# Kernel optimization log

Hardware: AMD Instinct MI355X
Metric: run time of the kernel (lower is better)

The kernel has to match this reference:

```python
import jax, jax.numpy as jnp
import numpy as np

B, S, T, H, F, V, OUT = 32, 40, 60, 256, 64, 50000, 128
D_IN = H + F  # LSTM input = input_size + feature_size (input_size == hidden_size)


def setup_inputs() -> dict:
    rng = np.random.default_rng(0)
    key = jax.random.key(0)
    ks = jax.random.split(key, 12)
    sc = 0.05
    # descending sentence counts per paragraph (pack_padded_sequence order), max == S
    lens = np.sort(rng.integers(1, S + 1, size=B))[::-1].copy()
    lens[0] = S
    # per-sentence token lengths; trailing (padding) sentences have length 0
    tok_len = rng.integers(1, T + 1, size=(B, S))
    tok_len = tok_len * (np.arange(S)[None, :] < lens[:, None])
    x_mask = jnp.asarray(np.arange(T)[None, None, :] >= tok_len[:, :, None])  # True = pad
    return {
        "x": jax.random.randint(ks[0], (B, S, T), 0, V),
        "x_mask": x_mask,
        "x_feature": jax.random.normal(ks[1], (B, S, T, F), jnp.float32),
        "sentences_len": jnp.asarray(lens, jnp.int32),
        "clause": jnp.zeros((B,), jnp.int32),
        "cls": jnp.zeros((B,), jnp.int32),
        "emb": jax.random.normal(ks[2], (V, H), jnp.float32) * 0.02,
        "attn_w": jax.random.normal(ks[3], (H,), jnp.float32) * sc,
        "attn_b": jnp.zeros((), jnp.float32),
        "wih_f": jax.random.normal(ks[4], (4 * H, D_IN), jnp.float32) * sc,
        "whh_f": jax.random.normal(ks[5], (4 * H, H), jnp.float32) * sc,
        "bih_f": jnp.zeros((4 * H,), jnp.float32),
        "bhh_f": jnp.zeros((4 * H,), jnp.float32),
        "wih_b": jax.random.normal(ks[6], (4 * H, D_IN), jnp.float32) * sc,
        "whh_b": jax.random.normal(ks[7], (4 * H, H), jnp.float32) * sc,
        "bih_b": jnp.zeros((4 * H,), jnp.float32),
        "bhh_b": jnp.zeros((4 * H,), jnp.float32),
        "fc_w": jax.random.normal(ks[8], (OUT, 2 * H), jnp.float32) * sc,
        "fc_b": jnp.zeros((OUT,), jnp.float32),
        "bn_gamma": jnp.ones((OUT,), jnp.float32),
        "bn_beta": jnp.zeros((OUT,), jnp.float32),
    }


def _lstm_last(X, m, wih, whh, bih, bhh, reverse):
    # X: (S, B, D) time-major inputs; m: (S, B) bool validity mask.
    # Masked update emulates pack_padded_sequence: carry freezes past each seq's length,
    # so the final carry equals torch's h_n for that direction.
    def step(carry, inp):
        h, c = carry
        xt, mt = inp
        g = xt @ wih.T + bih + h @ whh.T + bhh
        i, f, gg, o = jnp.split(g, 4, axis=-1)  # torch gate order i,f,g,o
        c2 = jax.nn.sigmoid(f) * c + jax.nn.sigmoid(i) * jnp.tanh(gg)
        h2 = jax.nn.sigmoid(o) * jnp.tanh(c2)
        upd = mt[:, None]
        return (jnp.where(upd, h2, h), jnp.where(upd, c2, c)), None

    nb, nh = X.shape[1], whh.shape[1]
    init = (jnp.zeros((nb, nh), X.dtype), jnp.zeros((nb, nh), X.dtype))
    (h, _), _ = jax.lax.scan(step, init, (X, m), reverse=reverse)
    return h


def _forward(x, x_mask, x_feature, sentences_len, emb, attn_w, attn_b,
             wih_f, whh_f, bih_f, bhh_f, wih_b, whh_b, bih_b, bhh_b,
             fc_w, fc_b, bn_gamma, bn_beta):
    e = emb[x]                                            # (B,S,T,H)
    valid_tok = ~x_mask                                   # (B,S,T)
    valid_sen = jnp.any(valid_tok, axis=-1)               # (B,S)
    score = jnp.einsum('bsth,h->bst', e, attn_w) + attn_b
    score = jnp.where(valid_tok, score, -jnp.inf)
    score = jnp.where(valid_sen[..., None], score, 0.0)   # avoid all-inf NaN rows
    alpha = jax.nn.relu(jax.nn.softmax(score, axis=-1))   # (B,S,T)
    alpha = jnp.where(valid_sen[..., None] & valid_tok, alpha, 0.0)
    emb_part = jnp.einsum('bst,bsth->bsh', alpha, e)      # attended sum over tokens
    feat_part = jnp.sum(x_feature * valid_tok[..., None].astype(x_feature.dtype), axis=2)
    sen = jnp.concatenate([emb_part, feat_part], axis=-1) # (B,S,H+F)
    sen = sen * valid_sen[..., None].astype(sen.dtype)    # empty sentences -> zero rows
    X = jnp.transpose(sen, (1, 0, 2))                     # (S,B,H+F) time-major
    m = jnp.arange(X.shape[0])[:, None] < sentences_len[None, :]  # (S,B)
    h_f = _lstm_last(X, m, wih_f, whh_f, bih_f, bhh_f, reverse=False)
    h_b = _lstm_last(X, m, wih_b, whh_b, bih_b, bhh_b, reverse=True)
    # torch: paragraph_hidden[0].view(batch, -1) on (2,B,H) = flat memory reinterpretation
    hidden = jnp.stack([h_f, h_b], axis=0).reshape(x.shape[0], -1)  # (B,2H)
    logits = hidden @ fc_w.T + fc_b                       # (B,OUT)
    mu = jnp.mean(logits, axis=0)
    var = jnp.mean((logits - mu) ** 2, axis=0)            # biased var (BN train mode)
    y = jax.nn.relu(bn_gamma * (logits - mu) / jnp.sqrt(var + 1e-5) + bn_beta)
    return jax.nn.log_softmax(y, axis=0)                  # original softmaxes over batch dim


def reference(x, x_mask, x_feature, sentences_len, clause, cls, emb, attn_w, attn_b,
              wih_f, whh_f, bih_f, bhh_f, wih_b, whh_b, bih_b, bhh_b,
              fc_w, fc_b, bn_gamma, bn_beta):
    # clause / cls are unused by the original forward
    return _forward(x, x_mask, x_feature, sentences_len, emb, attn_w, attn_b,
                    wih_f, whh_f, bih_f, bhh_f, wih_b, whh_b, bih_b, bhh_b,
                    fc_w, fc_b, bn_gamma, bn_beta)
```

## Files before the change

kernel.cpp:

```cpp
#include <hip/hip_runtime.h>
#include <stdint.h>

#define NB 32
#define NS 40
#define NT 60
#define NH 256
#define NF 64
#define NDIN 320
#define NG 1024
#define NSB 1280
#define NOUT 128

typedef __bf16 bf16x8 __attribute__((ext_vector_type(8)));
typedef float f32x4 __attribute__((ext_vector_type(4)));
typedef uint32_t u32x4 __attribute__((ext_vector_type(4)));

union bfrag { bf16x8 v; uint16_t u[8]; uint4 q; uint64_t d[2]; };
union f2arr { float2 v; float a[2]; };

__device__ __forceinline__ uint16_t f2bf(float f) {
  uint32_t u = __float_as_uint(f);
  u += 0x7fffu + ((u >> 16) & 1u);
  return (uint16_t)(u >> 16);
}
__device__ __forceinline__ float bf2f(uint16_t h) {
  return __uint_as_float(((uint32_t)h) << 16);
}
__device__ __forceinline__ float sig_fast(float x) { return 1.0f / (1.0f + __expf(-x)); }
__device__ __forceinline__ float tanh_fast(float x) {
  x = fminf(fmaxf(x, -15.0f), 15.0f);
  float t = __expf(2.0f * x);
  return (t - 1.0f) / (t + 1.0f);
}
__device__ __forceinline__ uint32_t ld_agent_u32(const uint32_t* p) {
  return __hip_atomic_load(p, __ATOMIC_RELAXED, __HIP_MEMORY_SCOPE_AGENT);
}

__global__ __launch_bounds__(256) void k_detect(const uint32_t* __restrict__ xm,
                                                int* __restrict__ flags,
                                                uint32_t* __restrict__ gr) {
  int bid = blockIdx.x, tid = threadIdx.x;
  {
    int gidx = bid * 256 + tid;
    u32x4 z = {0, 0, 0, 0};
    asm volatile("global_store_dwordx4 %0, %1, off sc1"
                 :: "v"((unsigned long long)(uintptr_t)(gr + (size_t)gidx * 4)), "v"(z)
                 : "memory");
  }
  __shared__ int s_notint, s_notflt;
  if (tid == 0) { s_notint = 0; s_notflt = 0; }
  __syncthreads();
  int notint = 0, notflt = 0;
  for (int i = bid * 600 + tid; i < (bid + 1) * 600; i += 256) {
    uint32_t v = xm[i];
    if (v > 1u) notint = 1;
    if (v != 0u && v != 0x3f800000u) notflt = 1;
  }
  if (notint) atomicOr(&s_notint, 1);
  if (notflt) atomicOr(&s_notflt, 1);
  __syncthreads();
  if (tid == 0) flags[8 + bid] = s_notint | (s_notflt << 1);
}

__global__ __launch_bounds__(256) void k_attn_prep(
    const int* __restrict__ x, const void* __restrict__ xmask,
    const float* __restrict__ xfeat, const int* __restrict__ slen,
    const float* __restrict__ emb, const float* __restrict__ attn_w,
    uint16_t* __restrict__ Xb, const int* __restrict__ flagp,
    const float* __restrict__ wf, const float* __restrict__ wb,
    uint16_t* __restrict__ outw)
{
  int tid = threadIdx.x;
  if (blockIdx.x >= 1280) {
    const int n = NG * NDIN;
    for (int idx = (blockIdx.x - 1280) * 256 + tid; idx < 2 * n; idx += 1280 * 256) {
      float v = (idx < n) ? wf[idx] : wb[idx - n];
      uint16_t hi = f2bf(v);
      outw[idx] = hi;
      outw[2 * n + idx] = f2bf(v - bf2f(hi));
    }
    return;
  }
  int bs = blockIdx.x;
  int b = bs / NS, s = bs % NS;
  uint16_t* Xh = Xb + (size_t)(s * NB + b) * NDIN;
  uint16_t* Xl = Xh + (size_t)NSB * NDIN;
  int len = slen[b];
  if (s >= len) {
    for (int i = tid; i < NDIN; i += 256) { Xh[i] = 0; Xl[i] = 0; }
    return;
  }
  __shared__ __attribute__((aligned(16))) float sw[NH];
  __shared__ float salpha[NT];
  __shared__ int sidx[NT];
  __shared__ unsigned char svalid[NT];
  __shared__ __attribute__((aligned(16))) uint16_t es[NT][NH];
  sw[tid] = attn_w[tid];
  int nv = 0;
  #pragma unroll
  for (int q = 0; q < 32; q++) nv |= flagp[8 + q];
  int flag = (!(nv & 1)) ? 0 : ((!(nv & 2)) ? 2 : 1);
  if (tid < NT) {
    int mi = bs * NT + tid;
    sidx[tid] = x[mi];
    int mv;
    if (flag == 1)      mv = ((const unsigned char*)xmask)[mi];
    else if (flag == 2) mv = (((const float*)xmask)[mi] != 0.0f) ? 1 : 0;
    else                mv = ((const int*)xmask)[mi];
    svalid[tid] = (mv == 0) ? 1 : 0;
  }
  __syncthreads();
  int wave = tid >> 6, lane = tid & 63;
  for (int t = wave; t < NT; t += 4) {
    float d = 0.0f;
    if (svalid[t]) {
      const float* er = emb + (size_t)sidx[t] * NH;
      float4 e4 = ((const float4*)er)[lane];
      float4 w4 = ((const float4*)sw)[lane];
      uint16_t* ed = &es[t][lane * 4];
      ed[0] = f2bf(e4.x); ed[1] = f2bf(e4.y); ed[2] = f2bf(e4.z); ed[3] = f2bf(e4.w);
      d = e4.x * w4.x + e4.y * w4.y + e4.z * w4.z + e4.w * w4.w;
      #pragma unroll
      for (int o = 32; o > 0; o >>= 1) d += __shfl_down(d, o);
    }
    if (lane == 0) salpha[t] = d;
  }
  __syncthreads();
  if (tid < 64) {
    int valid = (tid < NT) && svalid[tid];
    float v = valid ? salpha[tid] : -1e30f;
    float m = v;
    #pragma unroll
    for (int o = 32; o > 0; o >>= 1) m = fmaxf(m, __shfl_xor(m, o));
    float e = valid ? expf(v - m) : 0.0f;
    float ssum = e;
    #pragma unroll
    for (int o = 32; o > 0; o >>= 1) ssum += __shfl_xor(ssum, o);
    if (tid < NT) salpha[tid] = e / ssum;
  }
  __syncthreads();
  float acc = 0.0f;
  for (int t = 0; t < NT; t++) {
    float a = salpha[t];
    if (a != 0.0f) acc += a * bf2f(es[t][tid]);
  }
  {
    uint16_t hi = f2bf(acc);
    Xh[tid] = hi; Xl[tid] = f2bf(acc - bf2f(hi));
  }
  if (tid < NF) {
    float fa = 0.0f;
    const float* fp = xfeat + (size_t)bs * NT * NF + tid;
    for (int t = 0; t < NT; t++) if (svalid[t]) fa += fp[t * NF];
    uint16_t hi = f2bf(fa);
    Xh[NH + tid] = hi; Xl[NH + tid] = f2bf(fa - bf2f(hi));
  }
}

__global__ __launch_bounds__(512) void k_gbase(
    const uint16_t* __restrict__ Xb, const uint16_t* __restrict__ wihb,
    const float* __restrict__ bih_f, const float* __restrict__ bhh_f,
    const float* __restrict__ bih_b, const float* __restrict__ bhh_b,
    float* __restrict__ gbase)
{
  const int n = NG * NDIN;
  int wave = threadIdx.x >> 6, lane = threadIdx.x & 63;
  int job = blockIdx.x * 8 + wave;
  int dir = job / 1280;
  int r = job % 1280;
  int nt = r % 64, ms = r / 64;
  int m0 = ms * 64;
  const uint16_t* Wh = wihb + (size_t)dir * n;
  const uint16_t* Wl = Wh + (size_t)2 * n;
  const uint16_t* Ah = Xb;
  const uint16_t* Al = Xb + (size_t)NSB * NDIN;
  int lrow = lane & 15, lk = (lane >> 4) * 8;
  f32x4 acc0 = {0,0,0,0}, acc1 = acc0, acc2 = acc0, acc3 = acc0;
  for (int kk = 0; kk < 10; kk++) {
    int k0 = kk * 32 + lk;
    bfrag bh, bl, ah0, ah1, ah2, ah3, al0, al1, al2, al3;
    bh.q = *(const uint4*)(Wh + (size_t)(nt * 16 + lrow) * NDIN + k0);
    bl.q = *(const uint4*)(Wl + (size_t)(nt * 16 + lrow) * NDIN + k0);
    ah0.q = *(const uint4*)(Ah + (size_t)(m0 +  0 + lrow) * NDIN + k0);
    ah1.q = *(const uint4*)(Ah + (size_t)(m0 + 16 + lrow) * NDIN + k0);
    ah2.q = *(const uint4*)(Ah + (size_t)(m0 + 32 + lrow) * NDIN + k0);
    ah3.q = *(const uint4*)(Ah + (size_t)(m0 + 48 + lrow) * NDIN + k0);
    al0.q = *(const uint4*)(Al + (size_t)(m0 +  0 + lrow) * NDIN + k0);
    al1.q = *(const uint4*)(Al + (size_t)(m0 + 16 + lrow) * NDIN + k0);
    al2.q = *(const uint4*)(Al + (size_t)(m0 + 32 + lrow) * NDIN + k0);
    al3.q = *(const uint4*)(Al + (size_t)(m0 + 48 + lrow) * NDIN + k0);
    acc0 = __builtin_amdgcn_mfma_f32_16x16x32_bf16(ah0.v, bh.v, acc0, 0, 0, 0);
    acc0 = __builtin_amdgcn_mfma_f32_16x16x32_bf16(ah0.v, bl.v, acc0, 0, 0, 0);
    acc0 = __builtin_amdgcn_mfma_f32_16x16x32_bf16(al0.v, bh.v, acc0, 0, 0, 0);
    acc1 = __builtin_amdgcn_mfma_f32_16x16x32_bf16(ah1.v, bh.v, acc1, 0, 0, 0);
    acc1 = __builtin_amdgcn_mfma_f32_16x16x32_bf16(ah1.v, bl.v, acc1, 0, 0, 0);
    acc1 = __builtin_amdgcn_mfma_f32_16x16x32_bf16(al1.v, bh.v, acc1, 0, 0, 0);
    acc2 = __builtin_amdgcn_mfma_f32_16x16x32_bf16(ah2.v, bh.v, acc2, 0, 0, 0);
    acc2 = __builtin_amdgcn_mfma_f32_16x16x32_bf16(ah2.v, bl.v, acc2, 0, 0, 0);
    acc2 = __builtin_amdgcn_mfma_f32_16x16x32_bf16(al2.v, bh.v, acc2, 0, 0, 0);
    acc3 = __builtin_amdgcn_mfma_f32_16x16x32_bf16(ah3.v, bh.v, acc3, 0, 0, 0);
    acc3 = __builtin_amdgcn_mfma_f32_16x16x32_bf16(ah3.v, bl.v, acc3, 0, 0, 0);
    acc3 = __builtin_amdgcn_mfma_f32_16x16x32_bf16(al3.v, bh.v, acc3, 0, 0, 0);
  }
  int col = nt * 16 + lrow;
  float bias = dir ? (bih_b[col] + bhh_b[col]) : (bih_f[col] + bhh_f[col]);
  float* gb = gbase + (size_t)dir * NSB * NG;
  int rb = (lane >> 4) * 4;
  #pragma unroll
  for (int rr = 0; rr < 4; rr++) {
    gb[(size_t)(m0 +  0 + rb + rr) * NG + col] = acc0[rr] + bias;
    gb[(size_t)(m0 + 16 + rb + rr) * NG + col] = acc1[rr] + bias;
    gb[(size_t)(m0 + 32 + rb + rr) * NG + col] = acc2[rr] + bias;
    gb[(size_t)(m0 + 48 + rb + rr) * NG + col] = acc3[rr] + bias;
  }
}

__global__ __launch_bounds__(512, 2) void k_lstm(
    const float* __restrict__ whh_f_, const float* __restrict__ whh_b_,
    const float* __restrict__ gbase, const int* __restrict__ slen,
    uint32_t* __restrict__ gr)
{
  int wg = blockIdx.x;
  int dir = wg >> 3, p = wg & 7;
  int u0 = p * 32;
  int tid = threadIdx.x, wave = tid >> 6, lane = tid & 63;
  int lrow = lane & 15, lkb = (lane >> 4) * 8;
  const float* Wr = dir ? whh_b_ : whh_f_;
  const float* gb = gbase + (size_t)dir * NSB * NG;
  uint32_t* grd = gr + (size_t)dir * 2 * 64 * NB * 4;

  __shared__ __attribute__((aligned(16))) uint16_t hs[NB][264];
  __shared__ float tscr[8][32 * 18];

  bfrag wh[8];
  {
    int wr = (lrow >> 2) * 256 + u0 + wave * 4 + (lrow & 3);
    const float* wrow = Wr + (size_t)wr * NH;
    #pragma unroll
    for (int kk = 0; kk < 8; kk++) {
      int k0 = kk * 32 + lkb;
      bfrag th;
      #pragma unroll
      for (int e = 0; e < 8; e++) th.u[e] = f2bf(wrow[k0 + e]);
      wh[kk] = th;
    }
  }
  int beta = lane >> 1;
  int g64 = p * 8 + wave;
  int len = slen[beta];
  uint32_t hprev_hi = 0;
  float c0 = 0.0f, c1 = 0.0f;

  unsigned long long sa[2][4];
  #pragma unroll
  for (int par = 0; par < 2; par++) {
    const uint32_t* gpar = grd + (size_t)par * 64 * NB * 4;
    #pragma unroll
    for (int q = 0; q < 4; q++)
      sa[par][q] = (unsigned long long)(uintptr_t)(gpar + (size_t)(tid + q * 512) * 4);
  }

  for (int i = 0; i < NS; i++) {
    int t = dir ? (NS - 1 - i) : i;
    const float* gptr = gb + ((size_t)t * NB + beta) * NG + u0 + wave * 4 + (lane & 1) * 2;
    f2arr g0, g1, g2, g3;
    g0.v = *(const float2*)(gptr);
    g1.v = *(const float2*)(gptr + 256);
    g2.v = *(const float2*)(gptr + 512);
    g3.v = *(const float2*)(gptr + 768);
    u32x4 v0, v1, v2, v3;
    {
      const unsigned long long* a = sa[i & 1];
      uint32_t need = (uint32_t)i;
      long spins = 0;
      for (;;) {
        asm volatile(
          "global_load_dwordx4 %0, %4, off sc1\n\t"
          "global_load_dwordx4 %1, %5, off sc1\n\t"
          "global_load_dwordx4 %2, %6, off sc1\n\t"
          "global_load_dwordx4 %3, %7, off sc1\n\t"
          "s_waitcnt vmcnt(0)"
          : "=&v"(v0), "=&v"(v1), "=&v"(v2), "=&v"(v3)
          : "v"(a[0]), "v"(a[1]), "v"(a[2]), "v"(a[3])
          : "memory");
        if (v0.x >= need && v1.x >= need && v2.x >= need && v3.x >= need) break;
        if (++spins > (1L << 16)) break;
      }
    }
    __syncthreads();
    #pragma unroll
    for (int q = 0; q < 4; q++) {
      int s = tid + q * 512;
      int gq = s >> 5, bb = s & 31;
      u32x4 vv = (q == 0) ? v0 : (q == 1) ? v1 : (q == 2) ? v2 : v3;
      uint32_t* d = (uint32_t*)(&hs[bb][gq * 4]);
      d[0] = vv.y; d[1] = vv.z;
    }
    __syncthreads();
    f32x4 acc0 = {0,0,0,0}, acc1 = acc0;
    #pragma unroll
    for (int kk = 0; kk < 8; kk++) {
      int k0 = kk * 32 + lkb;
      bfrag ah0, ah1;
      ah0.q = *(const uint4*)(&hs[lrow][k0]);
      ah1.q = *(const uint4*)(&hs[16 + lrow][k0]);
      acc0 = __builtin_amdgcn_mfma_f32_16x16x32_bf16(ah0.v, wh[kk].v, acc0, 0, 0, 0);
      acc1 = __builtin_amdgcn_mfma_f32_16x16x32_bf16(ah1.v, wh[kk].v, acc1, 0, 0, 0);
    }
    volatile float* ts = &tscr[wave][0];
    {
      int colT = lane & 15, rb = (lane >> 4) * 4;
      #pragma unroll
      for (int rr = 0; rr < 4; rr++) {
        ts[(rb + rr) * 18 + colT]      = acc0[rr];
        ts[(16 + rb + rr) * 18 + colT] = acc1[rr];
      }
    }
    int e2 = (lane & 1) * 2;
    float gv00 = ts[beta * 18 + 0 + e2],  gv01 = ts[beta * 18 + 1 + e2];
    float gv10 = ts[beta * 18 + 4 + e2],  gv11 = ts[beta * 18 + 5 + e2];
    float gv20 = ts[beta * 18 + 8 + e2],  gv21 = ts[beta * 18 + 9 + e2];
    float gv30 = ts[beta * 18 + 12 + e2], gv31 = ts[beta * 18 + 13 + e2];
    {
      int upd = (t < len) ? 1 : 0;
      float gi0 = gv00 + g0.a[0], gi1 = gv01 + g0.a[1];
      float gf0 = gv10 + g1.a[0], gf1 = gv11 + g1.a[1];
      float gg0 = gv20 + g2.a[0], gg1 = gv21 + g2.a[1];
      float go0 = gv30 + g3.a[0], go1 = gv31 + g3.a[1];
      float c2a = sig_fast(gf0) * c0 + sig_fast(gi0) * tanh_fast(gg0);
      float c2b = sig_fast(gf1) * c1 + sig_fast(gi1) * tanh_fast(gg1);
      float h2a = sig_fast(go0) * tanh_fast(c2a);
      float h2b = sig_fast(go1) * tanh_fast(c2b);
      c0 = upd ? c2a : c0;
      c1 = upd ? c2b : c1;
      uint32_t hiw;
      if (upd) {
        uint16_t ha = f2bf(h2a), hbb = f2bf(h2b);
        hiw = (uint32_t)ha | ((uint32_t)hbb << 16);
      } else hiw = hprev_hi;
      hprev_hi = hiw;
      uint32_t hiw_p = __shfl_down(hiw, 1);
      if ((lane & 1) == 0) {
        uint32_t* gout = grd + ((size_t)(((i + 1) & 1) * 64 + g64) * NB + beta) * 4;
        u32x4 pv;
        pv.x = (uint32_t)(i + 1); pv.y = hiw; pv.z = hiw_p; pv.w = 0u;
        asm volatile("global_store_dwordx4 %0, %1, off sc1"
                     :: "v"((unsigned long long)(uintptr_t)gout), "v"(pv) : "memory");
      }
    }
  }
}

__global__ __launch_bounds__(512) void k_final(
    const uint32_t* __restrict__ gr, const float* __restrict__ fc_w,
    const float* __restrict__ fc_b, const float* __restrict__ gamma_,
    const float* __restrict__ beta_, float* __restrict__ outp)
{
  __shared__ float hid[NB][513];
  int tid = threadIdx.x;
  for (int idx = tid; idx < NB * 512; idx += 512) {
    int bb = idx >> 9, k = idx & 511;
    int bsrc = 2 * (bb & 15) + (k >> 8);
    int hcol = k & 255;
    int dirn = (bb < 16) ? 0 : 1;
    const uint32_t* g = gr + ((size_t)dirn * 2 * 64 * NB + (size_t)(hcol >> 2) * NB + bsrc) * 4;
    uint32_t w = ld_agent_u32(g + 1 + ((hcol >> 1) & 1));
    hid[bb][k] = bf2f((uint16_t)(w >> ((hcol & 1) * 16)));
  }
  __syncthreads();
  int wv = tid >> 6, lane = tid & 63;
  int o = blockIdx.x * 8 + wv;
  int b = lane >> 1, half = lane & 1;
  const float* wrow = fc_w + (size_t)o * 512 + half * 256;
  const float* hrow = &hid[b][half * 256];
  float part = 0.0f;
  #pragma unroll 8
  for (int j = 0; j < 256; j++) part += wrow[j] * hrow[j];
  part += __shfl_xor(part, 1);
  float y = part + fc_b[o];
  float s = y;
  #pragma unroll
  for (int off = 2; off < 64; off <<= 1) s += __shfl_xor(s, off);
  float mu = s * (1.0f / 32.0f);
  float d = y - mu;
  float v2 = d * d;
  #pragma unroll
  for (int off = 2; off < 64; off <<= 1) v2 += __shfl_xor(v2, off);
  float var = v2 * (1.0f / 32.0f);
  float gm = gamma_[o], be = beta_[o];
  float inv = 1.0f / sqrtf(var + 1e-5f);
  float yy = fmaxf(gm * (y - mu) * inv + be, 0.0f);
  float m = yy;
  #pragma unroll
  for (int off = 2; off < 64; off <<= 1) m = fmaxf(m, __shfl_xor(m, off));
  float e = expf(yy - m);
  float se = e;
  #pragma unroll
  for (int off = 2; off < 64; off <<= 1) se += __shfl_xor(se, off);
  float lse = m + logf(se);
  if (half == 0) outp[b * NOUT + o] = yy - lse;
}

extern "C" void kernel_launch(void* const* d_in, const int* in_sizes, int n_in,
                              void* d_out, int out_size, void* d_ws, size_t ws_size,
                              hipStream_t stream) {
  (void)in_sizes; (void)n_in; (void)out_size; (void)ws_size;
  const int*   x      = (const int*)  d_in[0];
  const void*  xmask  =               d_in[1];
  const float* xfeat  = (const float*)d_in[2];
  const int*   slen   = (const int*)  d_in[3];
  const float* emb    = (const float*)d_in[6];
  const float* attn_w = (const float*)d_in[7];
  const float* wih_f  = (const float*)d_in[9];
  const float* whh_f  = (const float*)d_in[10];
  const float* bih_f  = (const float*)d_in[11];
  const float* bhh_f  = (const float*)d_in[12];
  const float* wih_b  = (const float*)d_in[13];
  const float* whh_b  = (const float*)d_in[14];
  const float* bih_b  = (const float*)d_in[15];
  const float* bhh_b  = (const float*)d_in[16];
  const float* fc_w   = (const float*)d_in[17];
  const float* fc_b   = (const float*)d_in[18];
  const float* gam    = (const float*)d_in[19];
  const float* bet    = (const float*)d_in[20];

  char* ws = (char*)d_ws;
  int*      flags = (int*)ws;
  uint32_t* gr    = (uint32_t*)(ws + 4096);
  uint16_t* Xb    = (uint16_t*)(ws + 135168);
  uint16_t* wihb  = (uint16_t*)(ws + 1773568);
  float*    gbase = (float*)(ws + 4395008);

  k_detect<<<32, 256, 0, stream>>>((const uint32_t*)xmask, flags, gr);
  k_attn_prep<<<2560, 256, 0, stream>>>(x, xmask, xfeat, slen, emb, attn_w, Xb, flags,
                                        wih_f, wih_b, wihb);
  k_gbase<<<320, 512, 0, stream>>>(Xb, wihb, bih_f, bhh_f, bih_b, bhh_b, gbase);
  k_lstm<<<16, 512, 0, stream>>>(whh_f, whh_b, gbase, slen, gr);
  k_final<<<16, 512, 0, stream>>>(gr, fc_w, fc_b, gam, bet, (float*)d_out);
}
```

Measured before the change: 241.5 us.

## Fuse gate-precompute GEMM, LSTM recurrence and final head into one persistent kernel

Merges the input-projection GEMM, the bidirectional LSTM recurrence and the FC/BN/log-softmax head into one launch. The 16 recurrent blocks spin on per-row-tile counters that the GEMM blocks bump after storing their slice, so the recurrence can begin once its first timestep's gates are ready. The next step's gate values are also prefetched at the end of each step. This removes two launch gaps and overlaps the GEMM with the serial recurrence, at the cost of spin-waits with timeout escapes and a dependence on the 16 LSTM blocks being co-resident with the GEMM blocks.

```diff
diff --git a/kernel.cpp b/kernel.cpp
--- a/kernel.cpp
+++ b/kernel.cpp
@@ -35,9 +35,20 @@
 __device__ __forceinline__ uint32_t ld_agent_u32(const uint32_t* p) {
   return __hip_atomic_load(p, __ATOMIC_RELAXED, __HIP_MEMORY_SCOPE_AGENT);
 }
+__device__ __forceinline__ int ld_agent_int(const int* p) {
+  return __hip_atomic_load(p, __ATOMIC_RELAXED, __HIP_MEMORY_SCOPE_AGENT);
+}
+__device__ __forceinline__ void st_agent_f32(float* p, float v) {
+  __hip_atomic_store((uint32_t*)p, __float_as_uint(v), __ATOMIC_RELAXED, __HIP_MEMORY_SCOPE_AGENT);
+}
+__device__ __forceinline__ float2 lda_f2(const float* p) {
+  union { uint64_t u; float2 f; } c;
+  c.u = __hip_atomic_load((const uint64_t*)p, __ATOMIC_RELAXED, __HIP_MEMORY_SCOPE_AGENT);
+  return c.f;
+}
 
 __global__ __launch_bounds__(256) void k_detect(const uint32_t* __restrict__ xm,
-                                                int* __restrict__ flags,
+                                                int* __restrict__ ctrl,
                                                 uint32_t* __restrict__ gr) {
   int bid = blockIdx.x, tid = threadIdx.x;
   {
@@ -47,6 +58,7 @@
                  :: "v"((unsigned long long)(uintptr_t)(gr + (size_t)gidx * 4)), "v"(z)
                  : "memory");
   }
+  if (bid == 0 && tid < 64) ctrl[64 + tid] = 0;
   __shared__ int s_notint, s_notflt;
   if (tid == 0) { s_notint = 0; s_notflt = 0; }
   __syncthreads();
@@ -59,7 +71,7 @@
   if (notint) atomicOr(&s_notint, 1);
   if (notflt) atomicOr(&s_notflt, 1);
   __syncthreads();
-  if (tid == 0) flags[8 + bid] = s_notint | (s_notflt << 1);
+  if (tid == 0) ctrl[8 + bid] = s_notint | (s_notflt << 1);
 }
 
 __global__ __launch_bounds__(256) void k_attn_prep(
@@ -157,80 +169,86 @@
   }
 }
 
-__global__ __launch_bounds__(512) void k_gbase(
+__global__ __launch_bounds__(512, 2) void k_fused(
     const uint16_t* __restrict__ Xb, const uint16_t* __restrict__ wihb,
     const float* __restrict__ bih_f, const float* __restrict__ bhh_f,
     const float* __restrict__ bih_b, const float* __restrict__ bhh_b,
-    float* __restrict__ gbase)
+    const float* __restrict__ whh_f_, const float* __restrict__ whh_b_,
+    const int* __restrict__ slen, float* __restrict__ gbase,
+    uint32_t* __restrict__ gr, int* __restrict__ ctrl,
+    const float* __restrict__ fc_w, const float* __restrict__ fc_b,
+    const float* __restrict__ gamma_, const float* __restrict__ beta_,
+    float* __restrict__ outp)
 {
-  const int n = NG * NDIN;
-  int wave = threadIdx.x >> 6, lane = threadIdx.x & 63;
-  int job = blockIdx.x * 8 + wave;
-  int dir = job / 1280;
-  int r = job % 1280;
-  int nt = r % 64, ms = r / 64;
-  int m0 = ms * 64;
-  const uint16_t* Wh = wihb + (size_t)dir * n;
-  const uint16_t* Wl = Wh + (size_t)2 * n;
-  const uint16_t* Ah = Xb;
-  const uint16_t* Al = Xb + (size_t)NSB * NDIN;
-  int lrow = lane & 15, lk = (lane >> 4) * 8;
-  f32x4 acc0 = {0,0,0,0}, acc1 = acc0, acc2 = acc0, acc3 = acc0;
-  for (int kk = 0; kk < 10; kk++) {
-    int k0 = kk * 32 + lk;
-    bfrag bh, bl, ah0, ah1, ah2, ah3, al0, al1, al2, al3;
-    bh.q = *(const uint4*)(Wh + (size_t)(nt * 16 + lrow) * NDIN + k0);
-    bl.q = *(const uint4*)(Wl + (size_t)(nt * 16 + lrow) * NDIN + k0);
-    ah0.q = *(const uint4*)(Ah + (size_t)(m0 +  0 + lrow) * NDIN + k0);
-    ah1.q = *(const uint4*)(Ah + (size_t)(m0 + 16 + lrow) * NDIN + k0);
-    ah2.q = *(const uint4*)(Ah + (size_t)(m0 + 32 + lrow) * NDIN + k0);
-    ah3.q = *(const uint4*)(Ah + (size_t)(m0 + 48 + lrow) * NDIN + k0);
-    al0.q = *(const uint4*)(Al + (size_t)(m0 +  0 + lrow) * NDIN + k0);
-    al1.q = *(const uint4*)(Al + (size_t)(m0 + 16 + lrow) * NDIN + k0);
-    al2.q = *(const uint4*)(Al + (size_t)(m0 + 32 + lrow) * NDIN + k0);
-    al3.q = *(const uint4*)(Al + (size_t)(m0 + 48 + lrow) * NDIN + k0);
-    acc0 = __builtin_amdgcn_mfma_f32_16x16x32_bf16(ah0.v, bh.v, acc0, 0, 0, 0);
-    acc0 = __builtin_amdgcn_mfma_f32_16x16x32_bf16(ah0.v, bl.v, acc0, 0, 0, 0);
-    acc0 = __builtin_amdgcn_mfma_f32_16x16x32_bf16(al0.v, bh.v, acc0, 0, 0, 0);
-    acc1 = __builtin_amdgcn_mfma_f32_16x16x32_bf16(ah1.v, bh.v, acc1, 0, 0, 0);
-    acc1 = __builtin_amdgcn_mfma_f32_16x16x32_bf16(ah1.v, bl.v, acc1, 0, 0, 0);
-    acc1 = __builtin_amdgcn_mfma_f32_16x16x32_bf16(al1.v, bh.v, acc1, 0, 0, 0);
-    acc2 = __builtin_amdgcn_mfma_f32_16x16x32_bf16(ah2.v, bh.v, acc2, 0, 0, 0);
-    acc2 = __builtin_amdgcn_mfma_f32_16x16x32_bf16(ah2.v, bl.v, acc2, 0, 0, 0);
-    acc2 = __builtin_amdgcn_mfma_f32_16x16x32_bf16(al2.v, bh.v, acc2, 0, 0, 0);
-    acc3 = __builtin_amdgcn_mfma_f32_16x16x32_bf16(ah3.v, bh.v, acc3, 0, 0, 0);
-    acc3 = __builtin_amdgcn_mfma_f32_16x16x32_bf16(ah3.v, bl.v, acc3, 0, 0, 0);
-    acc3 = __builtin_amdgcn_mfma_f32_16x16x32_bf16(al3.v, bh.v, acc3, 0, 0, 0);
-  }
-  int col = nt * 16 + lrow;
-  float bias = dir ? (bih_b[col] + bhh_b[col]) : (bih_f[col] + bhh_f[col]);
-  float* gb = gbase + (size_t)dir * NSB * NG;
-  int rb = (lane >> 4) * 4;
-  #pragma unroll
-  for (int rr = 0; rr < 4; rr++) {
-    gb[(size_t)(m0 +  0 + rb + rr) * NG + col] = acc0[rr] + bias;
-    gb[(size_t)(m0 + 16 + rb + rr) * NG + col] = acc1[rr] + bias;
-    gb[(size_t)(m0 + 32 + rb + rr) * NG + col] = acc2[rr] + bias;
-    gb[(size_t)(m0 + 48 + rb + rr) * NG + col] = acc3[rr] + bias;
-  }
-}
-
-__global__ __launch_bounds__(512, 2) void k_lstm(
-    const float* __restrict__ whh_f_, const float* __restrict__ whh_b_,
-    const float* __restrict__ gbase, const int* __restrict__ slen,
-    uint32_t* __restrict__ gr)
-{
+  __shared__ __attribute__((aligned(16))) char smem_[65664];
+  int tid = threadIdx.x, wave = tid >> 6, lane = tid & 63;
+  int lrow = lane & 15, lkb = (lane >> 4) * 8;
+
+  if (blockIdx.x >= 16) {
+    const int n = NG * NDIN;
+    int job = (blockIdx.x - 16) * 8 + wave;
+    int dir = job / 1280;
+    int r = job % 1280;
+    int nt = r % 64, ms = r / 64;
+    int m0 = ms * 64;
+    const uint16_t* Wh = wihb + (size_t)dir * n;
+    const uint16_t* Wl = Wh + (size_t)2 * n;
+    const uint16_t* Ah = Xb;
+    const uint16_t* Al = Xb + (size_t)NSB * NDIN;
+    int lk = lkb;
+    f32x4 acc0 = {0,0,0,0}, acc1 = acc0, acc2 = acc0, acc3 = acc0;
+    for (int kk = 0; kk < 10; kk++) {
+      int k0 = kk * 32 + lk;
+      bfrag bh, bl, ah0, ah1, ah2, ah3, al0, al1, al2, al3;
+      bh.q = *(const uint4*)(Wh + (size_t)(nt * 16 + lrow) * NDIN + k0);
+      bl.q = *(const uint4*)(Wl + (size_t)(nt * 16 + lrow) * NDIN + k0);
+      ah0.q = *(const uint4*)(Ah + (size_t)(m0 +  0 + lrow) * NDIN + k0);
+      ah1.q = *(const uint4*)(Ah + (size_t)(m0 + 16 + lrow) * NDIN + k0);
+      ah2.q = *(const uint4*)(Ah + (size_t)(m0 + 32 + lrow) * NDIN + k0);
+      ah3.q = *(const uint4*)(Ah + (size_t)(m0 + 48 + lrow) * NDIN + k0);
+      al0.q = *(const uint4*)(Al + (size_t)(m0 +  0 + lrow) * NDIN + k0);
+      al1.q = *(const uint4*)(Al + (size_t)(m0 + 16 + lrow) * NDIN + k0);
+      al2.q = *(const uint4*)(Al + (size_t)(m0 + 32 + lrow) * NDIN + k0);
+      al3.q = *(const uint4*)(Al + (size_t)(m0 + 48 + lrow) * NDIN + k0);
+      acc0 = __builtin_amdgcn_mfma_f32_16x16x32_bf16(ah0.v, bh.v, acc0, 0, 0, 0);
+      acc0 = __builtin_amdgcn_mfma_f32_16x16x32_bf16(ah0.v, bl.v, acc0, 0, 0, 0);
+      acc0 = __builtin_amdgcn_mfma_f32_16x16x32_bf16(al0.v, bh.v, acc0, 0, 0, 0);
+      acc1 = __builtin_amdgcn_mfma_f32_16x16x32_bf16(ah1.v, bh.v, acc1, 0, 0, 0);
+      acc1 = __builtin_amdgcn_mfma_f32_16x16x32_bf16(ah1.v, bl.v, acc1, 0, 0, 0);
+      acc1 = __builtin_amdgcn_mfma_f32_16x16x32_bf16(al1.v, bh.v, acc1, 0, 0, 0);
+      acc2 = __builtin_amdgcn_mfma_f32_16x16x32_bf16(ah2.v, bh.v, acc2, 0, 0, 0);
+      acc2 = __builtin_amdgcn_mfma_f32_16x16x32_bf16(ah2.v, bl.v, acc2, 0, 0, 0);
+      acc2 = __builtin_amdgcn_mfma_f32_16x16x32_bf16(al2.v, bh.v, acc2, 0, 0, 0);
+      acc3 = __builtin_amdgcn_mfma_f32_16x16x32_bf16(ah3.v, bh.v, acc3, 0, 0, 0);
+      acc3 = __builtin_amdgcn_mfma_f32_16x16x32_bf16(ah3.v, bl.v, acc3, 0, 0, 0);
+      acc3 = __builtin_amdgcn_mfma_f32_16x16x32_bf16(al3.v, bh.v, acc3, 0, 0, 0);
+    }
+    int col = nt * 16 + lrow;
+    float bias = dir ? (bih_b[col] + bhh_b[col]) : (bih_f[col] + bhh_f[col]);
+    float* gb = gbase + (size_t)dir * NSB * NG;
+    int rb = (lane >> 4) * 4;
+    #pragma unroll
+    for (int rr = 0; rr < 4; rr++) {
+      st_agent_f32(&gb[(size_t)(m0 +  0 + rb + rr) * NG + col], acc0[rr] + bias);
+      st_agent_f32(&gb[(size_t)(m0 + 16 + rb + rr) * NG + col], acc1[rr] + bias);
+      st_agent_f32(&gb[(size_t)(m0 + 32 + rb + rr) * NG + col], acc2[rr] + bias);
+      st_agent_f32(&gb[(size_t)(m0 + 48 + rb + rr) * NG + col], acc3[rr] + bias);
+    }
+    asm volatile("s_waitcnt vmcnt(0)" ::: "memory");
+    if (lane == 0)
+      __hip_atomic_fetch_add(&ctrl[64 + dir * 32 + ms], 1,
+                             __ATOMIC_RELAXED, __HIP_MEMORY_SCOPE_AGENT);
+    return;
+  }
+
   int wg = blockIdx.x;
   int dir = wg >> 3, p = wg & 7;
   int u0 = p * 32;
-  int tid = threadIdx.x, wave = tid >> 6, lane = tid & 63;
-  int lrow = lane & 15, lkb = (lane >> 4) * 8;
   const float* Wr = dir ? whh_b_ : whh_f_;
   const float* gb = gbase + (size_t)dir * NSB * NG;
   uint32_t* grd = gr + (size_t)dir * 2 * 64 * NB * 4;
-
-  __shared__ __attribute__((aligned(16))) uint16_t hs[NB][264];
-  __shared__ float tscr[8][32 * 18];
+  uint16_t (*hs)[264] = (uint16_t(*)[264])smem_;
+  volatile float* ts = (volatile float*)(smem_ + 16896) + wave * 576;
 
   bfrag wh[8];
   {
@@ -260,14 +278,24 @@
       sa[par][q] = (unsigned long long)(uintptr_t)(gpar + (size_t)(tid + q * 512) * 4);
   }
 
+  uint32_t ready_mask = 0;
+  f2arr g0, g1, g2, g3;
+  {
+    int t0 = dir ? (NS - 1) : 0;
+    int ms0 = t0 >> 1;
+    long sp = 0;
+    while (ld_agent_int(&ctrl[64 + dir * 32 + ms0]) < 64) {
+      __builtin_amdgcn_s_sleep(2);
+      if (++sp > (1L << 20)) break;
+    }
+    ready_mask |= 1u << ms0;
+    const float* gptr = gb + ((size_t)t0 * NB + beta) * NG + u0 + wave * 4 + (lane & 1) * 2;
+    g0.v = lda_f2(gptr);       g1.v = lda_f2(gptr + 256);
+    g2.v = lda_f2(gptr + 512); g3.v = lda_f2(gptr + 768);
+  }
+
   for (int i = 0; i < NS; i++) {
     int t = dir ? (NS - 1 - i) : i;
-    const float* gptr = gb + ((size_t)t * NB + beta) * NG + u0 + wave * 4 + (lane & 1) * 2;
-    f2arr g0, g1, g2, g3;
-    g0.v = *(const float2*)(gptr);
-    g1.v = *(const float2*)(gptr + 256);
-    g2.v = *(const float2*)(gptr + 512);
-    g3.v = *(const float2*)(gptr + 768);
     u32x4 v0, v1, v2, v3;
     {
       const unsigned long long* a = sa[i & 1];
@@ -307,7 +335,6 @@
       acc0 = __builtin_amdgcn_mfma_f32_16x16x32_bf16(ah0.v, wh[kk].v, acc0, 0, 0, 0);
       acc1 = __builtin_amdgcn_mfma_f32_16x16x32_bf16(ah1.v, wh[kk].v, acc1, 0, 0, 0);
     }
-    volatile float* ts = &tscr[wave][0];
     {
       int colT = lane & 15, rb = (lane >> 4) * 4;
       #pragma unroll
@@ -348,16 +375,36 @@
                      :: "v"((unsigned long long)(uintptr_t)gout), "v"(pv) : "memory");
       }
     }
-  }
-}
-
-__global__ __launch_bounds__(512) void k_final(
-    const uint32_t* __restrict__ gr, const float* __restrict__ fc_w,
-    const float* __restrict__ fc_b, const float* __restrict__ gamma_,
-    const float* __restrict__ beta_, float* __restrict__ outp)
-{
-  __shared__ float hid[NB][513];
-  int tid = threadIdx.x;
+    if (i + 1 < NS) {
+      int tn = dir ? (NS - 2 - i) : (i + 1);
+      int msn = tn >> 1;
+      if (!(ready_mask & (1u << msn))) {
+        long sp = 0;
+        while (ld_agent_int(&ctrl[64 + dir * 32 + msn]) < 64) {
+          __builtin_amdgcn_s_sleep(2);
+          if (++sp > (1L << 20)) break;
+        }
+        ready_mask |= 1u << msn;
+      }
+      const float* gptr = gb + ((size_t)tn * NB + beta) * NG + u0 + wave * 4 + (lane & 1) * 2;
+      g0.v = lda_f2(gptr);       g1.v = lda_f2(gptr + 256);
+      g2.v = lda_f2(gptr + 512); g3.v = lda_f2(gptr + 768);
+    }
+  }
+
+  #pragma unroll
+  for (int q = 0; q < 8; q++) {
+    int s = tid + q * 512;
+    int d_ = s >> 11, r2 = s & 2047;
+    const uint32_t* ga = gr + ((size_t)d_ * 2 * 2048 + r2) * 4;
+    long sp = 0;
+    while (ld_agent_u32(ga) < (uint32_t)NS) {
+      __builtin_amdgcn_s_sleep(1);
+      if (++sp > (1L << 20)) break;
+    }
+  }
+  __syncthreads();
+  float* hid = (float*)smem_;
   for (int idx = tid; idx < NB * 512; idx += 512) {
     int bb = idx >> 9, k = idx & 511;
     int bsrc = 2 * (bb & 15) + (k >> 8);
@@ -365,23 +412,22 @@
     int dirn = (bb < 16) ? 0 : 1;
     const uint32_t* g = gr + ((size_t)dirn * 2 * 64 * NB + (size_t)(hcol >> 2) * NB + bsrc) * 4;
     uint32_t w = ld_agent_u32(g + 1 + ((hcol >> 1) & 1));
-    hid[bb][k] = bf2f((uint16_t)(w >> ((hcol & 1) * 16)));
-  }
-  __syncthreads();
-  int wv = tid >> 6, lane = tid & 63;
-  int o = blockIdx.x * 8 + wv;
+    hid[bb * 513 + k] = bf2f((uint16_t)(w >> ((hcol & 1) * 16)));
+  }
+  __syncthreads();
+  int o = blockIdx.x * 8 + wave;
   int b = lane >> 1, half = lane & 1;
   const float* wrow = fc_w + (size_t)o * 512 + half * 256;
-  const float* hrow = &hid[b][half * 256];
+  const float* hrow = &hid[b * 513 + half * 256];
   float part = 0.0f;
   #pragma unroll 8
   for (int j = 0; j < 256; j++) part += wrow[j] * hrow[j];
   part += __shfl_xor(part, 1);
   float y = part + fc_b[o];
-  float s = y;
-  #pragma unroll
-  for (int off = 2; off < 64; off <<= 1) s += __shfl_xor(s, off);
-  float mu = s * (1.0f / 32.0f);
+  float s2 = y;
+  #pragma unroll
+  for (int off = 2; off < 64; off <<= 1) s2 += __shfl_xor(s2, off);
+  float mu = s2 * (1.0f / 32.0f);
   float d = y - mu;
   float v2 = d * d;
   #pragma unroll
@@ -425,16 +471,16 @@
   const float* bet    = (const float*)d_in[20];
 
   char* ws = (char*)d_ws;
-  int*      flags = (int*)ws;
+  int*      ctrl  = (int*)ws;
   uint32_t* gr    = (uint32_t*)(ws + 4096);
   uint16_t* Xb    = (uint16_t*)(ws + 135168);
   uint16_t* wihb  = (uint16_t*)(ws + 1773568);
   float*    gbase = (float*)(ws + 4395008);
 
-  k_detect<<<32, 256, 0, stream>>>((const uint32_t*)xmask, flags, gr);
-  k_attn_prep<<<2560, 256, 0, stream>>>(x, xmask, xfeat, slen, emb, attn_w, Xb, flags,
+  k_detect<<<32, 256, 0, stream>>>((const uint32_t*)xmask, ctrl, gr);
+  k_attn_prep<<<2560, 256, 0, stream>>>(x, xmask, xfeat, slen, emb, attn_w, Xb, ctrl,
                                         wih_f, wih_b, wihb);
-  k_gbase<<<320, 512, 0, stream>>>(Xb, wihb, bih_f, bhh_f, bih_b, bhh_b, gbase);
-  k_lstm<<<16, 512, 0, stream>>>(whh_f, whh_b, gbase, slen, gr);
-  k_final<<<16, 512, 0, stream>>>(gr, fc_w, fc_b, gam, bet, (float*)d_out);
-}
+  k_fused<<<336, 512, 0, stream>>>(Xb, wihb, bih_f, bhh_f, bih_b, bhh_b,
+                                   whh_f, whh_b, slen, gbase, gr, ctrl,
+                                   fc_w, fc_b, gam, bet, (float*)d_out);
+}
```

Measured after the change: 292.9 us. 21.3% more time.
